# Performance work log

Hardware: AMD Instinct MI355X
Metric: run time of the kernel (lower is better)

## Reference

```python
import jax, jax.numpy as jnp
import numpy as np

NU, NI, NE, NR = 100000, 50000, 200000, 64
D, K, EDGES, L, B = 64, 16, 2000000, 2, 4096
REG = 1e-4


def setup_inputs() -> dict:
    key = jax.random.key(0)
    ks = jax.random.split(key, 18)
    f = lambda k, sh: jax.random.normal(k, sh, dtype=jnp.float32)
    return {
        # embedding tables (init std=0.01 as in the torch module)
        'user_emb_w': f(ks[0], (NU, D)) * 0.01,
        'item_emb_w': f(ks[1], (NI, D)) * 0.01,
        'entity_emb_w': f(ks[2], (NE, D)) * 0.01,
        'relation_emb_w': f(ks[3], (NR, D)) * 0.01,
        # per-layer linear params (stacked over L layers)
        'Wk_w': f(ks[4], (L, D, 2 * D)) * 0.05,
        'Wk_b': f(ks[5], (L, D)) * 0.05,
        'Wa_w': f(ks[6], (L, D, D)) * 0.05,
        'Wa_b': f(ks[7], (L, D)) * 0.05,
        'Wb_w': f(ks[8], (L, D, D)) * 0.05,
        'Wb_b': f(ks[9], (L, D)) * 0.05,
        'edge_norm': jax.random.uniform(ks[10], (EDGES,), dtype=jnp.float32),
        # BPR batch ids
        'user': jax.random.randint(ks[11], (B,), 0, NU, dtype=jnp.int32),
        'pos_item': jax.random.randint(ks[12], (B,), 0, NI, dtype=jnp.int32),
        'neg_item': jax.random.randint(ks[13], (B,), 0, NI, dtype=jnp.int32),
        # interaction graph edge lists
        'edge_u': jax.random.randint(ks[14], (EDGES,), 0, NU, dtype=jnp.int32),
        'edge_i': jax.random.randint(ks[15], (EDGES,), 0, NI, dtype=jnp.int32),
        # KG neighbors: K (relation, entity) pairs per item
        'kg_rel': jax.random.randint(ks[16], (NI, K), 0, NR, dtype=jnp.int32),
        'kg_ent': jax.random.randint(ks[17], (NI, K), 0, NE, dtype=jnp.int32),
    }


def reference(user_emb_w, item_emb_w, entity_emb_w, relation_emb_w,
              Wk_w, Wk_b, Wa_w, Wa_b, Wb_w, Wb_b, edge_norm,
              user, pos_item, neg_item, edge_u, edge_i, kg_rel, kg_ent):
    # KG neighbor gathers (entity/relation tables are constant across layers)
    v = entity_emb_w[kg_ent]        # [NI, K, D]
    r = relation_emb_w[kg_rel]      # [NI, K, D]
    norm = edge_norm[:, None]       # [E, 1]

    u_cur, i_cur = user_emb_w, item_emb_w
    u_sum, i_sum = user_emb_w, item_emb_w
    for l in range(L):
        # --- KG attention (vectorized over all items and neighbors) ---
        hv = v * i_cur[:, None, :]                            # [NI, K, D]
        # concat([hv, hv]) @ Wk.T == hv @ (Wk[:, :D] + Wk[:, D:]).T
        w_eff = Wk_w[l][:, :D] + Wk_w[l][:, D:]               # [D, D]
        proj = jnp.einsum('ikd,od->iko', hv, w_eff) + Wk_b[l]  # [NI, K, D]
        score = jax.nn.leaky_relu(jnp.sum(r * proj, axis=-1), 0.2)  # [NI, K]
        alpha = jax.nn.softmax(score, axis=-1)                # softmax over neighbors
        kg_item = jnp.einsum('ik,ikd->id', alpha, v)          # [NI, D]
        # --- LightGCN propagation (segment scatter-add) ---
        agg_i = jax.ops.segment_sum(norm * u_cur[edge_u], edge_i, num_segments=NI)
        agg_u = jax.ops.segment_sum(norm * i_cur[edge_i], edge_u, num_segments=NU)
        # --- Gated fusion ---
        gate = jax.nn.sigmoid(kg_item @ Wa_w[l].T + Wa_b[l]
                              + agg_i @ Wb_w[l].T + Wb_b[l])
        i_cur = gate * kg_item + (1.0 - gate) * agg_i
        u_cur = agg_u
        u_sum = u_sum + u_cur
        i_sum = i_sum + i_cur

    # --- BPR loss ---
    u_e = u_sum[user]
    pos_e = i_sum[pos_item]
    neg_e = i_sum[neg_item]
    pos_s = jnp.sum(u_e * pos_e, axis=-1)
    neg_s = jnp.sum(u_e * neg_e, axis=-1)
    bpr = -jnp.mean(jnp.log(jax.nn.sigmoid(pos_s - neg_s) + 1e-10))
    l2 = (jnp.sum(u_e ** 2) + jnp.sum(pos_e ** 2) + jnp.sum(neg_e ** 2)) / user.shape[0]
    return bpr + REG * l2
```

## Files before the change

### kernel.cpp

```cpp
#include <hip/hip_runtime.h>
#include <math.h>

constexpr int DD    = 64;
constexpr int KK    = 16;
constexpr int NUs   = 100000;
constexpr int NIs   = 50000;
constexpr int NEs   = 200000;
constexpr int NRs   = 64;
constexpr int NEDGE = 2000000;
constexpr int LAYERS = 2;
constexpr int BB    = 4096;
constexpr float REGf = 1e-4f;

constexpr int SUBB  = 256;
constexpr int NB_I  = (NIs + SUBB - 1) / SUBB;
constexpr int NB_U  = (NUs + SUBB - 1) / SUBB;
constexpr int NBT   = NB_I + NB_U;
constexpr int CH    = 8192;
constexpr int NCHK  = (NEDGE + CH - 1) / CH;

__device__ __forceinline__ float wave_sum_f(float x) {
#pragma unroll
  for (int off = 32; off > 0; off >>= 1) x += __shfl_xor(x, off);
  return x;
}


__global__ __launch_bounds__(256) void bhist_kernel(const int* __restrict__ edge_u,
                                                    const int* __restrict__ edge_i,
                                                    int* __restrict__ gbkt) {
  __shared__ int lcnt[NBT];
  for (int b = threadIdx.x; b < NBT; b += 256) lcnt[b] = 0;
  __syncthreads();
  int base = blockIdx.x * CH;
  for (int k = threadIdx.x; k < CH; k += 256) {
    int e = base + k;
    if (e < NEDGE) {
      atomicAdd(&lcnt[edge_i[e] >> 8], 1);
      atomicAdd(&lcnt[NB_I + (edge_u[e] >> 8)], 1);
    }
  }
  __syncthreads();
  for (int b = threadIdx.x; b < NBT; b += 256) {
    int c = lcnt[b];
    if (c) atomicAdd(&gbkt[b], c);
  }
}

__global__ __launch_bounds__(1024) void bscan_kernel(const int* __restrict__ gbkt,
                                                     int* __restrict__ bktbase,
                                                     int* __restrict__ bktcur,
                                                     int* rp_i, int* rp_u) {
  __shared__ int sv[1024];
  int tid = threadIdx.x;
  int x = (tid < NBT) ? gbkt[tid] : 0;
  bool segU = (tid >= NB_I);
  int v = x;
  sv[tid] = v;
  __syncthreads();
  for (int off = 1; off < 1024; off <<= 1) {
    int y = 0;
    if (tid >= off) {
      int o = tid - off;
      if ((o >= NB_I) == segU) y = sv[o];
    }
    __syncthreads();
    v += y;
    sv[tid] = v;
    __syncthreads();
  }
  if (tid < NBT) {
    int ex = v - x;
    bktbase[tid] = ex;
    bktcur[tid] = ex;
  }
  if (tid == 0) { rp_i[NIs] = NEDGE; rp_u[NUs] = NEDGE; }
}

__global__ __launch_bounds__(256) void bscatter_kernel(const int* __restrict__ edge_u,
                                                       const int* __restrict__ edge_i,
                                                       const float* __restrict__ enorm,
                                                       int* __restrict__ bktcur,
                                                       int2* __restrict__ tmp_i,
                                                       int2* __restrict__ tmp_u) {
  __shared__ int lcnt[NBT];
  __shared__ int lbase[NBT];
  for (int b = threadIdx.x; b < NBT; b += 256) lcnt[b] = 0;
  __syncthreads();
  int base = blockIdx.x * CH;
  for (int k = threadIdx.x; k < CH; k += 256) {
    int e = base + k;
    if (e < NEDGE) {
      atomicAdd(&lcnt[edge_i[e] >> 8], 1);
      atomicAdd(&lcnt[NB_I + (edge_u[e] >> 8)], 1);
    }
  }
  __syncthreads();
  for (int b = threadIdx.x; b < NBT; b += 256) {
    int c = lcnt[b];
    lbase[b] = c ? atomicAdd(&bktcur[b], c) : 0;
    lcnt[b] = 0;
  }
  __syncthreads();
  for (int k = threadIdx.x; k < CH; k += 256) {
    int e = base + k;
    if (e < NEDGE) {
      int it = edge_i[e], u = edge_u[e];
      int wb = __float_as_int(enorm[e]);
      int bi = it >> 8;
      int p = lbase[bi] + atomicAdd(&lcnt[bi], 1);
      tmp_i[p] = make_int2(((it & 255) << 20) | u, wb);
      int bu = NB_I + (u >> 8);
      int q = lbase[bu] + atomicAdd(&lcnt[bu], 1);
      tmp_u[q] = make_int2(((u & 255) << 20) | it, wb);
    }
  }
}

__global__ __launch_bounds__(256) void bsort_kernel(const int* __restrict__ gbkt,
                                                    const int* __restrict__ bktbase,
                                                    const int2* __restrict__ tmp_i,
                                                    const int2* __restrict__ tmp_u,
                                                    int2* __restrict__ pair_i,
                                                    int2* __restrict__ pair_u,
                                                    int* __restrict__ rp_i,
                                                    int* __restrict__ rp_u) {
  int b = blockIdx.x;
  bool isI = (b < NB_I);
  const int2* tmp = isI ? tmp_i : tmp_u;
  int2* po = isI ? pair_i : pair_u;
  int* rp = isI ? rp_i : rp_u;
  int ndst = isI ? NIs : NUs;
  int localb = isI ? b : b - NB_I;
  int start = bktbase[b];
  int size = gbkt[b];
  __shared__ int dcnt[256];
  __shared__ int dpos[256];
  __shared__ int wt[4];
  int tid = threadIdx.x;
  dcnt[tid] = 0;
  __syncthreads();
  for (int k = tid; k < size; k += 256) atomicAdd(&dcnt[tmp[start + k].x >> 20], 1);
  __syncthreads();
  int c = dcnt[tid];
  int lane = tid & 63, wid = tid >> 6;
  int v = c;
#pragma unroll
  for (int off = 1; off < 64; off <<= 1) {
    int y = __shfl_up(v, off);
    if (lane >= off) v += y;
  }
  if (lane == 63) wt[wid] = v;
  __syncthreads();
  int woff = 0;
#pragma unroll
  for (int w = 0; w < 4; ++w)
    if (w < wid) woff += wt[w];
  int excl = woff + v - c;
  dpos[tid] = excl;
  int idx = localb * 256 + tid;
  if (idx < ndst) rp[idx] = start + excl;
  dcnt[tid] = 0;
  __syncthreads();
  for (int k = tid; k < size; k += 256) {
    int2 pw = tmp[start + k];
    int sub = pw.x >> 20;
    int j = dpos[sub] + atomicAdd(&dcnt[sub], 1);
    po[start + j] = make_int2(pw.x & 0xFFFFF, pw.y);
  }
}

__global__ __launch_bounds__(64) void rt_kernel(const float* __restrict__ RE,
                                                const float* __restrict__ Wkw,
                                                const float* __restrict__ Wkb,
                                                float* Rt, float* cvec) {
  int l = blockIdx.x >> 6;
  int n = blockIdx.x & 63;
  int d = threadIdx.x;
  const float* W  = Wkw + (size_t)l * DD * 2 * DD;
  const float* re = RE + n * DD;
  float acc = 0.f;
  for (int o = 0; o < DD; ++o) {
    float w = W[o * 2 * DD + d] + W[o * 2 * DD + DD + d];
    acc += re[o] * w;
  }
  Rt[(l * NRs + n) * DD + d] = acc;
  float p = re[d] * Wkb[l * DD + d];
  p = wave_sum_f(p);
  if (d == 0) cvec[l * NRs + n] = p;
}

__global__ __launch_bounds__(256) void attn_kernel(const float* __restrict__ EE,
                                                   const float* __restrict__ Rt_l,
                                                   const float* __restrict__ c_l,
                                                   const int* __restrict__ kg_ent,
                                                   const int* __restrict__ kg_rel,
                                                   const float* __restrict__ i_cur,
                                                   float* __restrict__ kg_item) {
  __shared__ float rt_s[NRs * DD];
  __shared__ float c_s[NRs];
  for (int m = threadIdx.x; m < NRs * DD; m += blockDim.x) rt_s[m] = Rt_l[m];
  for (int m = threadIdx.x; m < NRs; m += blockDim.x) c_s[m] = c_l[m];
  __syncthreads();
  int lane = threadIdx.x & 63;
  int wid = threadIdx.x >> 6;
  int wpg = gridDim.x * (blockDim.x >> 6);
  for (int i = blockIdx.x * (blockDim.x >> 6) + wid; i < NIs; i += wpg) {
    float icur = i_cur[i * DD + lane];
    int eidx = 0, ridx = 0;
    if (lane < KK) { eidx = kg_ent[i * KK + lane]; ridx = kg_rel[i * KK + lane]; }
    float vk[KK];
    float sc[KK];
#pragma unroll
    for (int k = 0; k < KK; ++k) {
      int ent = __shfl(eidx, k);
      int rel = __shfl(ridx, k);
      float v = EE[ent * DD + lane];
      vk[k] = v;
      float p = v * icur * rt_s[rel * DD + lane];
      p = wave_sum_f(p);
      float s = p + c_s[rel];
      sc[k] = (s >= 0.f) ? s : 0.2f * s;
    }
    float m = sc[0];
#pragma unroll
    for (int k = 1; k < KK; ++k) m = fmaxf(m, sc[k]);
    float ssum = 0.f;
#pragma unroll
    for (int k = 0; k < KK; ++k) { sc[k] = __expf(sc[k] - m); ssum += sc[k]; }
    float inv = 1.f / ssum;
    float kg = 0.f;
#pragma unroll
    for (int k = 0; k < KK; ++k) kg += sc[k] * inv * vk[k];
    kg_item[i * DD + lane] = kg;
  }
}

__global__ __launch_bounds__(256) void agg2_kernel(
    const int* __restrict__ rp_i, const int2* __restrict__ pair_i,
    const float* __restrict__ embU, float* __restrict__ aggi,
    const int* __restrict__ rp_u, const int2* __restrict__ pair_u,
    const float* __restrict__ embI, float* __restrict__ unext,
    float* __restrict__ usum, const float* __restrict__ usum_init) {
  int lane = threadIdx.x & 63;
  int wid  = threadIdx.x >> 6;
  int sub  = lane & 15;
  int grp  = lane >> 4;
  int wpg  = gridDim.x * (blockDim.x >> 6);
  const int total = NIs + NUs;
  for (int row = blockIdx.x * (blockDim.x >> 6) + wid; row < total; row += wpg) {
    bool isU = row >= NIs;
    int r = isU ? (row - NIs) : row;
    const int*  rp = isU ? rp_u   : rp_i;
    const int2* pr = isU ? pair_u : pair_i;
    const float* emb = isU ? embI : embU;
    int s0 = rp[r], s1 = rp[r + 1];
    float ax0 = 0.f, ay0 = 0.f, az0 = 0.f, aw0 = 0.f;
    float ax1 = 0.f, ay1 = 0.f, az1 = 0.f, aw1 = 0.f;
    for (int base = s0; base < s1; base += 64) {
      int lim = s1 - base; if (lim > 64) lim = 64;
      int sj = 0; float wj = 0.f;
      if (lane < lim) {
        int2 pw = pr[base + lane];
        sj = pw.x; wj = __int_as_float(pw.y);
      }
      for (int j = 0; j < lim; j += 8) {
        int m0 = j + grp;
        int m1 = j + 4 + grp;
        int   a0 = __shfl(sj, m0); float q0 = __shfl(wj, m0);
        int   a1 = __shfl(sj, m1); float q1 = __shfl(wj, m1);
        float4 e0 = reinterpret_cast<const float4*>(emb + ((size_t)a0 << 6))[sub];
        float4 e1 = reinterpret_cast<const float4*>(emb + ((size_t)a1 << 6))[sub];
        ax0 += q0 * e0.x; ay0 += q0 * e0.y; az0 += q0 * e0.z; aw0 += q0 * e0.w;
        ax1 += q1 * e1.x; ay1 += q1 * e1.y; az1 += q1 * e1.z; aw1 += q1 * e1.w;
      }
    }
    float ax = ax0 + ax1, ay = ay0 + ay1, az = az0 + az1, aw = aw0 + aw1;
    ax += __shfl_xor(ax, 16); ay += __shfl_xor(ay, 16);
    az += __shfl_xor(az, 16); aw += __shfl_xor(aw, 16);
    ax += __shfl_xor(ax, 32); ay += __shfl_xor(ay, 32);
    az += __shfl_xor(az, 32); aw += __shfl_xor(aw, 32);
    if (lane < 16) {
      float4 o; o.x = ax; o.y = ay; o.z = az; o.w = aw;
      if (!isU) {
        reinterpret_cast<float4*>(aggi + ((size_t)r << 6))[sub] = o;
      } else {
        reinterpret_cast<float4*>(unext + ((size_t)r << 6))[sub] = o;
        float4 si;
        if (usum_init) si = reinterpret_cast<const float4*>(usum_init + ((size_t)r << 6))[sub];
        else           si = reinterpret_cast<float4*>(usum + ((size_t)r << 6))[sub];
        float4 s; s.x = si.x + ax; s.y = si.y + ay; s.z = si.z + az; s.w = si.w + aw;
        reinterpret_cast<float4*>(usum + ((size_t)r << 6))[sub] = s;
      }
    }
  }
}

__global__ __launch_bounds__(256) void gate_kernel(const float* __restrict__ Wa,
                                                   const float* __restrict__ Wab,
                                                   const float* __restrict__ Wb,
                                                   const float* __restrict__ Wbb,
                                                   const float* __restrict__ kg_item,
                                                   const float* __restrict__ agg_i,
                                                   const float* __restrict__ i_sum_init,
                                                   float* __restrict__ i_next,
                                                   float* __restrict__ i_sum) {
  __shared__ float at[DD * 65];
  __shared__ float bt[DD * 65];
  for (int m = threadIdx.x; m < DD * DD; m += blockDim.x) {
    int o = m >> 6, d = m & 63;
    at[d * 65 + o] = Wa[m];
    bt[d * 65 + o] = Wb[m];
  }
  __syncthreads();
  int lane = threadIdx.x & 63, wid = threadIdx.x >> 6;
  int wpg = gridDim.x * (blockDim.x >> 6);
  float wab = Wab[lane], wbb = Wbb[lane];
  for (int i = blockIdx.x * (blockDim.x >> 6) + wid; i < NIs; i += wpg) {
    float kg = kg_item[i * DD + lane];
    float ag = agg_i[i * DD + lane];
    float acca = 0.f, accb = 0.f;
#pragma unroll
    for (int d = 0; d < DD; ++d) {
      float kd = __shfl(kg, d);
      float ad = __shfl(ag, d);
      acca += kd * at[d * 65 + lane];
      accb += ad * bt[d * 65 + lane];
    }
    float g = 1.f / (1.f + __expf(-(acca + wab + accb + wbb)));
    float inew = g * kg + (1.f - g) * ag;
    i_next[i * DD + lane] = inew;
    if (i_sum_init) i_sum[i * DD + lane] = i_sum_init[i * DD + lane] + inew;
    else            i_sum[i * DD + lane] += inew;
  }
}

__global__ __launch_bounds__(256) void loss_kernel(const float* __restrict__ u_sum,
                                                   const float* __restrict__ i_sum,
                                                   const int* __restrict__ user,
                                                   const int* __restrict__ pos,
                                                   const int* __restrict__ neg,
                                                   float* acc) {
  int lane = threadIdx.x & 63, wid = threadIdx.x >> 6;
  int wpg = gridDim.x * (blockDim.x >> 6);
  float lacc = 0.f, l2acc = 0.f;
  for (int b = blockIdx.x * (blockDim.x >> 6) + wid; b < BB; b += wpg) {
    float u = u_sum[user[b] * DD + lane];
    float p = i_sum[pos[b] * DD + lane];
    float n = i_sum[neg[b] * DD + lane];
    float ps = wave_sum_f(u * p);
    float ns = wave_sum_f(u * n);
    float sq = wave_sum_f(u * u + p * p + n * n);
    if (lane == 0) {
      float x = ps - ns;
      float sig = 1.f / (1.f + expf(-x));
      lacc += logf(sig + 1e-10f);
      l2acc += sq;
    }
  }
  if (lane == 0) {
    atomicAdd(&acc[0], lacc);
    atomicAdd(&acc[1], l2acc);
  }
}

__global__ void final_kernel(const float* acc, float* out) {
  out[0] = -acc[0] / (float)BB + REGf * (acc[1] / (float)BB);
}


extern "C" void kernel_launch(void* const* d_in, const int* in_sizes, int n_in,
                              void* d_out, int out_size, void* d_ws, size_t ws_size,
                              hipStream_t stream) {
  const float* UE   = (const float*)d_in[0];
  const float* IE   = (const float*)d_in[1];
  const float* EE   = (const float*)d_in[2];
  const float* RE   = (const float*)d_in[3];
  const float* Wkw  = (const float*)d_in[4];
  const float* Wkb  = (const float*)d_in[5];
  const float* Waw  = (const float*)d_in[6];
  const float* Wab  = (const float*)d_in[7];
  const float* Wbw  = (const float*)d_in[8];
  const float* Wbb  = (const float*)d_in[9];
  const float* enorm = (const float*)d_in[10];
  const int* user   = (const int*)d_in[11];
  const int* pos    = (const int*)d_in[12];
  const int* neg    = (const int*)d_in[13];
  const int* edge_u = (const int*)d_in[14];
  const int* edge_i = (const int*)d_in[15];
  const int* kg_rel = (const int*)d_in[16];
  const int* kg_ent = (const int*)d_in[17];

  size_t off = 0;
  char* base = (char*)d_ws;
  auto take = [&](size_t bytes) -> void* {
    void* p = base + off;
    off += (bytes + 255) & ~(size_t)255;
    return p;
  };
  float* Rt      = (float*)take(LAYERS * NRs * DD * sizeof(float));
  float* cvec    = (float*)take(LAYERS * NRs * sizeof(float));
  float* acc     = (float*)take(8 * sizeof(float));
  int*   gbkt    = (int*)take(NBT * sizeof(int));
  int*   bktbase = (int*)take(NBT * sizeof(int));
  int*   bktcur  = (int*)take(NBT * sizeof(int));
  int*   rp_i    = (int*)take((NIs + 1) * sizeof(int));
  int*   rp_u    = (int*)take((NUs + 1) * sizeof(int));
  int2*  tmp_i   = (int2*)take((size_t)NEDGE * sizeof(int2));
  int2*  tmp_u   = (int2*)take((size_t)NEDGE * sizeof(int2));
  int2*  pair_i  = (int2*)take((size_t)NEDGE * sizeof(int2));
  int2*  pair_u  = (int2*)take((size_t)NEDGE * sizeof(int2));
  float* kg      = (float*)take((size_t)NIs * DD * sizeof(float));
  float* aggi    = (float*)take((size_t)NIs * DD * sizeof(float));
  float* iA      = (float*)take((size_t)NIs * DD * sizeof(float));
  float* iB      = (float*)take((size_t)NIs * DD * sizeof(float));
  float* isum    = (float*)take((size_t)NIs * DD * sizeof(float));
  float* uA      = (float*)take((size_t)NUs * DD * sizeof(float));
  float* uB      = (float*)take((size_t)NUs * DD * sizeof(float));
  float* usum    = (float*)take((size_t)NUs * DD * sizeof(float));
  (void)ws_size; (void)in_sizes; (void)n_in; (void)out_size;

  hipMemsetAsync(gbkt, 0, NBT * sizeof(int), stream);
  hipMemsetAsync(acc, 0, 8 * sizeof(float), stream);

  bhist_kernel<<<NCHK, 256, 0, stream>>>(edge_u, edge_i, gbkt);
  bscan_kernel<<<1, 1024, 0, stream>>>(gbkt, bktbase, bktcur, rp_i, rp_u);
  bscatter_kernel<<<NCHK, 256, 0, stream>>>(edge_u, edge_i, enorm, bktcur, tmp_i, tmp_u);
  bsort_kernel<<<NBT, 256, 0, stream>>>(gbkt, bktbase, tmp_i, tmp_u,
                                        pair_i, pair_u, rp_i, rp_u);
  rt_kernel<<<LAYERS * NRs, 64, 0, stream>>>(RE, Wkw, Wkb, Rt, cvec);

  const float* u_cur = UE;
  const float* i_cur = IE;
  float* unext[2] = {uA, uB};
  float* inext[2] = {iA, iB};
  for (int l = 0; l < LAYERS; ++l) {
    attn_kernel<<<2048, 256, 0, stream>>>(EE, Rt + l * NRs * DD, cvec + l * NRs,
                                          kg_ent, kg_rel, i_cur, kg);
    agg2_kernel<<<2048, 256, 0, stream>>>(rp_i, pair_i, u_cur, aggi,
                                          rp_u, pair_u, i_cur, unext[l],
                                          usum, (l == 0) ? UE : nullptr);
    gate_kernel<<<2048, 256, 0, stream>>>(Waw + (size_t)l * DD * DD, Wab + l * DD,
                                          Wbw + (size_t)l * DD * DD, Wbb + l * DD,
                                          kg, aggi, (l == 0) ? IE : nullptr,
                                          inext[l], isum);
    u_cur = unext[l];
    i_cur = inext[l];
  }

  loss_kernel<<<1024, 256, 0, stream>>>(usum, isum, user, pos, neg, acc);
  final_kernel<<<1, 1, 0, stream>>>(acc, (float*)d_out);
}
```

Measured before the change: 1.027 ms.

## Map one 16-lane group per row in attention and aggregation kernels

Both the KG attention kernel and the CSR aggregation kernel now assign one 16-lane subgroup, with float4 per lane, to each item or user row instead of a full 64-lane wavefront. The attention kernel drops its shared-memory copy of the relation table and reads it straight from global memory, and the dot-product reduction falls from a 6-step to a 4-step shuffle. The aggregation kernel processes edges in chunks of 16 with padded zero weights and drops the cross-group reduction. The aim is better lane utilization for short rows (about 20 to 40 edges, 16 neighbors) and wider vector loads; the cost is more register pressure from the float4 vk array and redundant padded loads when a row's edge count is not a multiple of 16.

Measured after the change: 941.1 us. -8.4%, faster.

```diff
diff --git a/kernel.cpp b/kernel.cpp
--- a/kernel.cpp
+++ b/kernel.cpp
@@ -197,29 +197,31 @@
                                                    const int* __restrict__ kg_rel,
                                                    const float* __restrict__ i_cur,
                                                    float* __restrict__ kg_item) {
-  __shared__ float rt_s[NRs * DD];
-  __shared__ float c_s[NRs];
-  for (int m = threadIdx.x; m < NRs * DD; m += blockDim.x) rt_s[m] = Rt_l[m];
-  for (int m = threadIdx.x; m < NRs; m += blockDim.x) c_s[m] = c_l[m];
-  __syncthreads();
-  int lane = threadIdx.x & 63;
-  int wid = threadIdx.x >> 6;
-  int wpg = gridDim.x * (blockDim.x >> 6);
-  for (int i = blockIdx.x * (blockDim.x >> 6) + wid; i < NIs; i += wpg) {
-    float icur = i_cur[i * DD + lane];
-    int eidx = 0, ridx = 0;
-    if (lane < KK) { eidx = kg_ent[i * KK + lane]; ridx = kg_rel[i * KK + lane]; }
-    float vk[KK];
+  int tid = threadIdx.x;
+  int l16 = tid & 15;
+  int gbase = ((tid & 63) >> 4) << 4;
+  int gid = blockIdx.x * 16 + (tid >> 4);
+  int ngrp = gridDim.x * 16;
+  for (int i = gid; i < NIs; i += ngrp) {
+    float4 ic = reinterpret_cast<const float4*>(i_cur + ((size_t)i << 6))[l16];
+    int ent = kg_ent[i * KK + l16];
+    int rel = kg_rel[i * KK + l16];
+    float4 vk[KK];
+#pragma unroll
+    for (int k = 0; k < KK; ++k) {
+      int e = __shfl(ent, gbase + k);
+      vk[k] = reinterpret_cast<const float4*>(EE + ((size_t)e << 6))[l16];
+    }
     float sc[KK];
 #pragma unroll
     for (int k = 0; k < KK; ++k) {
-      int ent = __shfl(eidx, k);
-      int rel = __shfl(ridx, k);
-      float v = EE[ent * DD + lane];
-      vk[k] = v;
-      float p = v * icur * rt_s[rel * DD + lane];
-      p = wave_sum_f(p);
-      float s = p + c_s[rel];
+      int rl = __shfl(rel, gbase + k);
+      float4 rt = reinterpret_cast<const float4*>(Rt_l + ((size_t)rl << 6))[l16];
+      float p = vk[k].x * ic.x * rt.x + vk[k].y * ic.y * rt.y
+              + vk[k].z * ic.z * rt.z + vk[k].w * ic.w * rt.w;
+      p += __shfl_xor(p, 1); p += __shfl_xor(p, 2);
+      p += __shfl_xor(p, 4); p += __shfl_xor(p, 8);
+      float s = p + c_l[rl];
       sc[k] = (s >= 0.f) ? s : 0.2f * s;
     }
     float m = sc[0];
@@ -229,10 +231,14 @@
 #pragma unroll
     for (int k = 0; k < KK; ++k) { sc[k] = __expf(sc[k] - m); ssum += sc[k]; }
     float inv = 1.f / ssum;
-    float kg = 0.f;
-#pragma unroll
-    for (int k = 0; k < KK; ++k) kg += sc[k] * inv * vk[k];
-    kg_item[i * DD + lane] = kg;
+    float4 o = make_float4(0.f, 0.f, 0.f, 0.f);
+#pragma unroll
+    for (int k = 0; k < KK; ++k) {
+      float a = sc[k] * inv;
+      o.x += a * vk[k].x; o.y += a * vk[k].y;
+      o.z += a * vk[k].z; o.w += a * vk[k].w;
+    }
+    reinterpret_cast<float4*>(kg_item + ((size_t)i << 6))[l16] = o;
   }
 }
 
@@ -242,56 +248,51 @@
     const int* __restrict__ rp_u, const int2* __restrict__ pair_u,
     const float* __restrict__ embI, float* __restrict__ unext,
     float* __restrict__ usum, const float* __restrict__ usum_init) {
-  int lane = threadIdx.x & 63;
-  int wid  = threadIdx.x >> 6;
-  int sub  = lane & 15;
-  int grp  = lane >> 4;
-  int wpg  = gridDim.x * (blockDim.x >> 6);
+  int tid = threadIdx.x;
+  int l16 = tid & 15;
+  int gbase = ((tid & 63) >> 4) << 4;
+  int gid = blockIdx.x * 16 + (tid >> 4);
+  int ngrp = gridDim.x * 16;
   const int total = NIs + NUs;
-  for (int row = blockIdx.x * (blockDim.x >> 6) + wid; row < total; row += wpg) {
+  for (int row = gid; row < total; row += ngrp) {
     bool isU = row >= NIs;
     int r = isU ? (row - NIs) : row;
     const int*  rp = isU ? rp_u   : rp_i;
     const int2* pr = isU ? pair_u : pair_i;
     const float* emb = isU ? embI : embU;
     int s0 = rp[r], s1 = rp[r + 1];
-    float ax0 = 0.f, ay0 = 0.f, az0 = 0.f, aw0 = 0.f;
-    float ax1 = 0.f, ay1 = 0.f, az1 = 0.f, aw1 = 0.f;
-    for (int base = s0; base < s1; base += 64) {
-      int lim = s1 - base; if (lim > 64) lim = 64;
+    float4 accA = make_float4(0.f, 0.f, 0.f, 0.f);
+    float4 accB = make_float4(0.f, 0.f, 0.f, 0.f);
+    for (int base = s0; base < s1; base += 16) {
+      int lim = s1 - base;
       int sj = 0; float wj = 0.f;
-      if (lane < lim) {
-        int2 pw = pr[base + lane];
+      if (l16 < lim) {
+        int2 pw = pr[base + l16];
         sj = pw.x; wj = __int_as_float(pw.y);
       }
-      for (int j = 0; j < lim; j += 8) {
-        int m0 = j + grp;
-        int m1 = j + 4 + grp;
-        int   a0 = __shfl(sj, m0); float q0 = __shfl(wj, m0);
-        int   a1 = __shfl(sj, m1); float q1 = __shfl(wj, m1);
-        float4 e0 = reinterpret_cast<const float4*>(emb + ((size_t)a0 << 6))[sub];
-        float4 e1 = reinterpret_cast<const float4*>(emb + ((size_t)a1 << 6))[sub];
-        ax0 += q0 * e0.x; ay0 += q0 * e0.y; az0 += q0 * e0.z; aw0 += q0 * e0.w;
-        ax1 += q1 * e1.x; ay1 += q1 * e1.y; az1 += q1 * e1.z; aw1 += q1 * e1.w;
+#pragma unroll
+      for (int jj = 0; jj < 8; ++jj) {
+        int aA = __shfl(sj, gbase + jj);     float qA = __shfl(wj, gbase + jj);
+        int aB = __shfl(sj, gbase + 8 + jj); float qB = __shfl(wj, gbase + 8 + jj);
+        float4 eA = reinterpret_cast<const float4*>(emb + ((size_t)aA << 6))[l16];
+        float4 eB = reinterpret_cast<const float4*>(emb + ((size_t)aB << 6))[l16];
+        accA.x += qA * eA.x; accA.y += qA * eA.y; accA.z += qA * eA.z; accA.w += qA * eA.w;
+        accB.x += qB * eB.x; accB.y += qB * eB.y; accB.z += qB * eB.z; accB.w += qB * eB.w;
       }
     }
-    float ax = ax0 + ax1, ay = ay0 + ay1, az = az0 + az1, aw = aw0 + aw1;
-    ax += __shfl_xor(ax, 16); ay += __shfl_xor(ay, 16);
-    az += __shfl_xor(az, 16); aw += __shfl_xor(aw, 16);
-    ax += __shfl_xor(ax, 32); ay += __shfl_xor(ay, 32);
-    az += __shfl_xor(az, 32); aw += __shfl_xor(aw, 32);
-    if (lane < 16) {
-      float4 o; o.x = ax; o.y = ay; o.z = az; o.w = aw;
-      if (!isU) {
-        reinterpret_cast<float4*>(aggi + ((size_t)r << 6))[sub] = o;
-      } else {
-        reinterpret_cast<float4*>(unext + ((size_t)r << 6))[sub] = o;
-        float4 si;
-        if (usum_init) si = reinterpret_cast<const float4*>(usum_init + ((size_t)r << 6))[sub];
-        else           si = reinterpret_cast<float4*>(usum + ((size_t)r << 6))[sub];
-        float4 s; s.x = si.x + ax; s.y = si.y + ay; s.z = si.z + az; s.w = si.w + aw;
-        reinterpret_cast<float4*>(usum + ((size_t)r << 6))[sub] = s;
-      }
+    float4 o;
+    o.x = accA.x + accB.x; o.y = accA.y + accB.y;
+    o.z = accA.z + accB.z; o.w = accA.w + accB.w;
+    if (!isU) {
+      reinterpret_cast<float4*>(aggi + ((size_t)r << 6))[l16] = o;
+    } else {
+      reinterpret_cast<float4*>(unext + ((size_t)r << 6))[l16] = o;
+      float4 si;
+      if (usum_init) si = reinterpret_cast<const float4*>(usum_init + ((size_t)r << 6))[l16];
+      else           si = reinterpret_cast<float4*>(usum + ((size_t)r << 6))[l16];
+      float4 s;
+      s.x = si.x + o.x; s.y = si.y + o.y; s.z = si.z + o.z; s.w = si.w + o.w;
+      reinterpret_cast<float4*>(usum + ((size_t)r << 6))[l16] = s;
     }
   }
 }
```
